# Performance work log

Measured on AMD Instinct MI355X. Metric: run time of the kernel, lower is better.

The kernel has to match this reference:

```python
import jax, jax.numpy as jnp
import numpy as np

NODE_DIM = 256
HID = 128
EDGE_DIM = 128
NUM_BINS = 22
MAX_LEN = 2056
TOTAL_FEATS = HID * 3 + NUM_BINS * 2 + 2


def get_index_embedding(indices, embed_size, max_len):
    # sinusoidal index embedding as in RiboFlow utils
    K = jnp.arange(embed_size // 2, dtype=jnp.float32)
    ang = indices[..., None].astype(jnp.float32) * jnp.pi / (max_len ** (2.0 * K / embed_size))
    return jnp.concatenate([jnp.sin(ang), jnp.cos(ang)], axis=-1)


def calc_distogram(pos, min_bin, max_bin, num_bins):
    # pos: [B, N, 3] -> one-hot distogram [B, N, N, num_bins]
    d = jnp.linalg.norm(pos[:, :, None, :] - pos[:, None, :, :], axis=-1)[..., None]
    lower = jnp.linspace(min_bin, max_bin, num_bins)
    upper = jnp.concatenate([lower[1:], jnp.array([1e8], dtype=jnp.float32)])
    return ((d > lower) & (d < upper)).astype(jnp.float32)


def cross_concat(f):
    # f: [B, N, D] -> [B, N, N, 2D] via row/col tiling
    B, N, D = f.shape
    return jnp.concatenate([
        jnp.broadcast_to(f[:, :, None, :], (B, N, N, D)),
        jnp.broadcast_to(f[:, None, :, :], (B, N, N, D)),
    ], axis=-1)


def _linear_params(key, fi, fo):
    s = 1.0 / np.sqrt(fi)
    kw, kb = jax.random.split(key)
    W = jax.random.uniform(kw, (fi, fo), jnp.float32, -s, s)
    b = jax.random.uniform(kb, (fo,), jnp.float32, -s, s)
    return W, b


def setup_inputs() -> dict:
    key = jax.random.key(0)
    ks = jax.random.split(key, 12)
    B, N = 1, 512
    inp = {
        'node_features': jax.random.normal(ks[0], (B, N, NODE_DIM), jnp.float32),
        'trans': jax.random.normal(ks[1], (B, N, 3), jnp.float32) * 10.0,
        'sc_trans': jax.random.normal(ks[2], (B, N, 3), jnp.float32) * 10.0,
        'edge_mask': jnp.ones((B, N, N), jnp.float32),
        'flow_mask': (jax.random.uniform(ks[4], (B, N)) > 0.5).astype(jnp.float32),
    }
    inp['W_n2e'], inp['b_n2e'] = _linear_params(ks[5], NODE_DIM, HID)
    inp['W_rp'], inp['b_rp'] = _linear_params(ks[6], HID, HID)
    inp['W1'], inp['b1'] = _linear_params(ks[7], TOTAL_FEATS, EDGE_DIM)
    inp['W2'], inp['b2'] = _linear_params(ks[8], EDGE_DIM, EDGE_DIM)
    inp['W3'], inp['b3'] = _linear_params(ks[9], EDGE_DIM, EDGE_DIM)
    inp['ln_g'] = jnp.ones((EDGE_DIM,), jnp.float32)
    inp['ln_b'] = jnp.zeros((EDGE_DIM,), jnp.float32)
    return inp


def reference(node_features, trans, sc_trans, edge_mask, flow_mask,
              W_n2e, b_n2e, W_rp, b_rp, W1, b1, W2, b2, W3, b3, ln_g, ln_b):
    B, N, _ = node_features.shape
    # node -> edge projection, then cross-concat tiling: [B,N,N,2*HID]
    n2e = node_features @ W_n2e + b_n2e
    pair_node_feats = cross_concat(n2e)
    # relative position sinusoidal embedding + linear: [B,N,N,HID]
    seq = jnp.arange(N, dtype=jnp.float32)
    relpos = jnp.broadcast_to(seq[None, :, None] - seq[None, None, :], (B, N, N))
    relpos_feats = get_index_embedding(relpos, HID, MAX_LEN) @ W_rp + b_rp
    # distograms: [B,N,N,NUM_BINS] each
    dist_feats = calc_distogram(trans, 0.001, 20.0, NUM_BINS)
    sc_feats = calc_distogram(sc_trans, 0.001, 20.0, NUM_BINS)
    # flow mask pair features: [B,N,N,2]
    flow_feat = cross_concat(flow_mask[..., None])
    feats = jnp.concatenate([pair_node_feats, relpos_feats, dist_feats, sc_feats, flow_feat], axis=-1)
    # 3-layer MLP + LayerNorm
    h = jax.nn.relu(feats @ W1 + b1)
    h = jax.nn.relu(h @ W2 + b2)
    h = h @ W3 + b3
    mu = jnp.mean(h, axis=-1, keepdims=True)
    var = jnp.var(h, axis=-1, keepdims=True)
    h = (h - mu) * jax.lax.rsqrt(var + 1e-5) * ln_g + ln_b
    return h * edge_mask[..., None]
```

## Files before the change

kernel.cpp:

```cpp
#include <hip/hip_runtime.h>


using bf16x8 = __attribute__((ext_vector_type(8))) short;
using f32x4  = __attribute__((ext_vector_type(4))) float;

__device__ __forceinline__ unsigned short f2bf(float f) {
    unsigned int u;
    __builtin_memcpy(&u, &f, 4);
    unsigned int r = (u + 0x7fffu + ((u >> 16) & 1u)) >> 16;
    return (unsigned short)r;
}

__global__ void pre_node(const float* __restrict__ nf,
                         const float* __restrict__ Wn2e,
                         const float* __restrict__ bn2e,
                         const float* __restrict__ W1,
                         const float* __restrict__ b1,
                         const float* __restrict__ flow,
                         float* __restrict__ A, float* __restrict__ Bv)
{
    __shared__ float nfs[256];
    __shared__ float n2s[128];
    const int i = blockIdx.x, f = threadIdx.x;
    nfs[f]       = nf[i * 256 + f];
    nfs[f + 128] = nf[i * 256 + 128 + f];
    __syncthreads();
    float acc = bn2e[f];
    for (int k = 0; k < 256; k++) acc += nfs[k] * Wn2e[k * 128 + f];
    n2s[f] = acc;
    __syncthreads();
    const float fl = flow[i];
    float aA = b1[f] + fl * W1[428 * 128 + f];
    float aB =         fl * W1[429 * 128 + f];
    for (int k = 0; k < 128; k++) {
        const float s = n2s[k];
        aA += s * W1[k * 128 + f];
        aB += s * W1[(128 + k) * 128 + f];
    }
    A[i * 128 + f]  = aA;
    Bv[i * 128 + f] = aB;
}

__global__ void pre_rel(const float* __restrict__ Wrp,
                        const float* __restrict__ brp,
                        const float* __restrict__ W1,
                        float* __restrict__ Rm)
{
    __shared__ float emb[128];
    __shared__ float rp[128];
    const int dix = blockIdx.x;
    const float d = (float)(dix - 511);
    const int m = threadIdx.x;
    const int K = m & 63;
    const float denom = powf(2056.0f, (float)K * (1.0f / 64.0f));
    const float ang = d * 3.14159265358979323846f / denom;
    emb[m] = (m < 64) ? sinf(ang) : cosf(ang);
    __syncthreads();
    float acc = brp[m];
    for (int k = 0; k < 128; k++) acc += emb[k] * Wrp[k * 128 + m];
    rp[m] = acc;
    __syncthreads();
    float acc2 = 0.0f;
    for (int k = 0; k < 128; k++) acc2 += rp[k] * W1[(256 + k) * 128 + m];
    Rm[dix * 128 + m] = acc2;
}

__global__ __launch_bounds__(512, 2) void edge_main(
    const float* __restrict__ trans,
    const float* __restrict__ sctrans,
    const float* __restrict__ emask,
    const float* __restrict__ W1,
    const float* __restrict__ W2,
    const float* __restrict__ b2,
    const float* __restrict__ W3,
    const float* __restrict__ b3,
    const float* __restrict__ lng,
    const float* __restrict__ lnb,
    const float* __restrict__ A,
    const float* __restrict__ Bv,
    const float* __restrict__ Rm,
    float* __restrict__ out)
{
    __shared__ __align__(16) short W2L[16 * 128 * 8];
    __shared__ __align__(16) short W3L[16 * 128 * 8];
    __shared__ __align__(16) short hbuf[256 * 136];
    __shared__ __align__(16) float As[128];
    __shared__ int binsD[256];
    __shared__ int binsS[256];

    const int tid = threadIdx.x;
    const int i  = blockIdx.x >> 1;
    const int j0 = (blockIdx.x & 1) << 8;

    for (int idx = tid; idx < 16384; idx += 512) {
        const int k = idx >> 7, n = idx & 127;
        const int dst = ((k >> 3) * 128 + n) * 8 + (k & 7);
        W2L[dst] = (short)f2bf(W2[idx]);
        W3L[dst] = (short)f2bf(W3[idx]);
    }
    if (tid < 128) As[tid] = A[i * 128 + tid];

    {
        const int p = tid & 255;
        const float* P = (tid < 256) ? trans : sctrans;
        const int j = j0 + p;
        const float dx = __fsub_rn(P[i * 3 + 0], P[j * 3 + 0]);
        const float dy = __fsub_rn(P[i * 3 + 1], P[j * 3 + 1]);
        const float dz = __fsub_rn(P[i * 3 + 2], P[j * 3 + 2]);
        const float d2 = __fadd_rn(__fadd_rn(__fmul_rn(dx, dx), __fmul_rn(dy, dy)),
                                   __fmul_rn(dz, dz));
        const double dd = (double)sqrtf(d2);
        const double step = (20.0 - 0.001) / 21.0;
        int bin = -1;
        for (int b = 0; b < 22; b++) {
            const double lo = (b == 21) ? 20.0 : __dadd_rn(0.001, __dmul_rn((double)b, step));
            const double up = (b == 20) ? 20.0 :
                              ((b == 21) ? 1e8 : __dadd_rn(0.001, __dmul_rn((double)(b + 1), step)));
            if (dd > lo && dd < up) bin = b;
        }
        if (tid < 256) binsD[p] = bin; else binsS[p] = bin;
    }
    __syncthreads();

    const int w = tid >> 6;
    const int l = tid & 63;
    const int q = l >> 4;
    const int ln16 = l & 15;

    for (int it = 0; it < 16; it++) {
        const int flat = it * 64 + l;
        const int p = 32 * w + (flat >> 5);
        const int f = (flat & 31) << 2;
        const int j = j0 + p;
        const int didx = i - j + 511;
        const f32x4 bv = *(const f32x4*)&Bv[j * 128 + f];
        const f32x4 r  = *(const f32x4*)&Rm[didx * 128 + f];
        const f32x4 a  = *(const f32x4*)&As[f];
        const int bD = binsD[p], bS = binsS[p];
        const float sD = bD >= 0 ? 1.0f : 0.0f;
        const float sS = bS >= 0 ? 1.0f : 0.0f;
        const int rD = 384 + (bD >= 0 ? bD : 0);
        const int rS = 406 + (bS >= 0 ? bS : 0);
        const f32x4 wd  = *(const f32x4*)&W1[rD * 128 + f];
        const f32x4 wsv = *(const f32x4*)&W1[rS * 128 + f];
        float h0 = a.x + bv.x + r.x + sD * wd.x + sS * wsv.x;
        float h1 = a.y + bv.y + r.y + sD * wd.y + sS * wsv.y;
        float h2 = a.z + bv.z + r.z + sD * wd.z + sS * wsv.z;
        float h3 = a.w + bv.w + r.w + sD * wd.w + sS * wsv.w;
        h0 = fmaxf(h0, 0.0f); h1 = fmaxf(h1, 0.0f);
        h2 = fmaxf(h2, 0.0f); h3 = fmaxf(h3, 0.0f);
        uint2 pk;
        pk.x = (unsigned int)f2bf(h0) | ((unsigned int)f2bf(h1) << 16);
        pk.y = (unsigned int)f2bf(h2) | ((unsigned int)f2bf(h3) << 16);
        *(uint2*)&hbuf[p * 136 + f] = pk;
    }
    __syncthreads();

    bf16x8 af[2][4];
    for (int mt = 0; mt < 2; mt++)
        for (int kb = 0; kb < 4; kb++)
            af[mt][kb] = *(const bf16x8*)&hbuf[(32 * w + mt * 16 + ln16) * 136 + q * 8 + kb * 32];

    const f32x4 vzero = {0.0f, 0.0f, 0.0f, 0.0f};
    f32x4 acc[2][8];
    for (int mt = 0; mt < 2; mt++)
        for (int nb = 0; nb < 8; nb++) acc[mt][nb] = vzero;

    for (int nb = 0; nb < 8; nb++) {
        for (int kb = 0; kb < 4; kb++) {
            const bf16x8 bfrg = *(const bf16x8*)&W2L[((kb * 4 + q) * 128 + nb * 16 + ln16) * 8];
            acc[0][nb] = __builtin_amdgcn_mfma_f32_16x16x32_bf16(af[0][kb], bfrg, acc[0][nb], 0, 0, 0);
            acc[1][nb] = __builtin_amdgcn_mfma_f32_16x16x32_bf16(af[1][kb], bfrg, acc[1][nb], 0, 0, 0);
        }
    }
    __syncthreads();

    float b2v[8];
    for (int nb = 0; nb < 8; nb++) b2v[nb] = b2[nb * 16 + ln16];
    for (int nb = 0; nb < 8; nb++)
        for (int mt = 0; mt < 2; mt++)
            for (int rg = 0; rg < 4; rg++) {
                float v = acc[mt][nb][rg] + b2v[nb];
                v = fmaxf(v, 0.0f);
                const int p = 32 * w + mt * 16 + q * 4 + rg;
                hbuf[p * 136 + nb * 16 + ln16] = (short)f2bf(v);
            }
    __syncthreads();

    for (int mt = 0; mt < 2; mt++)
        for (int kb = 0; kb < 4; kb++)
            af[mt][kb] = *(const bf16x8*)&hbuf[(32 * w + mt * 16 + ln16) * 136 + q * 8 + kb * 32];
    for (int mt = 0; mt < 2; mt++)
        for (int nb = 0; nb < 8; nb++) acc[mt][nb] = vzero;
    for (int nb = 0; nb < 8; nb++) {
        for (int kb = 0; kb < 4; kb++) {
            const bf16x8 bfrg = *(const bf16x8*)&W3L[((kb * 4 + q) * 128 + nb * 16 + ln16) * 8];
            acc[0][nb] = __builtin_amdgcn_mfma_f32_16x16x32_bf16(af[0][kb], bfrg, acc[0][nb], 0, 0, 0);
            acc[1][nb] = __builtin_amdgcn_mfma_f32_16x16x32_bf16(af[1][kb], bfrg, acc[1][nb], 0, 0, 0);
        }
    }

    float b3v[8], gv[8], bbv[8];
    for (int nb = 0; nb < 8; nb++) {
        const int n = nb * 16 + ln16;
        b3v[nb] = b3[n];
        gv[nb]  = lng[n];
        bbv[nb] = lnb[n];
    }
    for (int mt = 0; mt < 2; mt++) {
        for (int rg = 0; rg < 4; rg++) {
            float v[8];
            float s = 0.0f;
            for (int nb = 0; nb < 8; nb++) { v[nb] = acc[mt][nb][rg] + b3v[nb]; s += v[nb]; }
            for (int m = 1; m < 16; m <<= 1) s += __shfl_xor(s, m, 64);
            const float mu = s * (1.0f / 128.0f);
            float ss = 0.0f;
            for (int nb = 0; nb < 8; nb++) { const float dv = v[nb] - mu; ss += dv * dv; }
            for (int m = 1; m < 16; m <<= 1) ss += __shfl_xor(ss, m, 64);
            const float rstd = rsqrtf(ss * (1.0f / 128.0f) + 1e-5f);
            const int p = 32 * w + mt * 16 + q * 4 + rg;
            const int j = j0 + p;
            const float msk = emask[i * 512 + j];
            const int obase = (i * 512 + j) * 128;
            for (int nb = 0; nb < 8; nb++) {
                const float o = ((v[nb] - mu) * rstd * gv[nb] + bbv[nb]) * msk;
                out[obase + nb * 16 + ln16] = o;
            }
        }
    }
}

extern "C" void kernel_launch(void* const* d_in, const int* in_sizes, int n_in,
                              void* d_out, int out_size, void* d_ws, size_t ws_size,
                              hipStream_t stream)
{
    const float* nf    = (const float*)d_in[0];
    const float* trans = (const float*)d_in[1];
    const float* sctr  = (const float*)d_in[2];
    const float* emask = (const float*)d_in[3];
    const float* flow  = (const float*)d_in[4];
    const float* Wn2e  = (const float*)d_in[5];
    const float* bn2e  = (const float*)d_in[6];
    const float* Wrp   = (const float*)d_in[7];
    const float* brp   = (const float*)d_in[8];
    const float* W1    = (const float*)d_in[9];
    const float* b1    = (const float*)d_in[10];
    const float* W2    = (const float*)d_in[11];
    const float* b2    = (const float*)d_in[12];
    const float* W3    = (const float*)d_in[13];
    const float* b3    = (const float*)d_in[14];
    const float* lng   = (const float*)d_in[15];
    const float* lnb   = (const float*)d_in[16];

    float* ws = (float*)d_ws;
    float* A  = ws;
    float* Bv = ws + 512 * 128;
    float* Rm = ws + 2 * 512 * 128;
    float* out = (float*)d_out;

    pre_node<<<512, 128, 0, stream>>>(nf, Wn2e, bn2e, W1, b1, flow, A, Bv);
    pre_rel<<<1023, 128, 0, stream>>>(Wrp, brp, W1, Rm);
    edge_main<<<1024, 512, 0, stream>>>(trans, sctr, emask, W1, W2, b2, W3, b3,
                                        lng, lnb, A, Bv, Rm, out);
}
```

Measured before the change: 260.5 us.

## Precast W2/W3 to bf16 once, read from global, drop block syncs

Moves the per-block fp32-to-bf16 conversion and swizzle of W2/W3 into a merged precompute kernel, so edge_main reads pre-swizzled bf16 weights from global memory instead of staging them in LDS. The freed LDS and a per-warp row ownership that removes __syncthreads allow more blocks per CU (launch bounds raised to 4). It also merges the two pre kernels into one launch, replaces the 22-iteration double bin loop with a direct computation, and uses cheaper round-half-up bf16 packing. The direct bin formula and the rounding change may differ from the reference at bin edges.

After: 267.3 us. 2.6% more time.

```diff
diff --git a/kernel.cpp b/kernel.cpp
--- a/kernel.cpp
+++ b/kernel.cpp
@@ -4,138 +4,142 @@
 using bf16x8 = __attribute__((ext_vector_type(8))) short;
 using f32x4  = __attribute__((ext_vector_type(4))) float;
 
-__device__ __forceinline__ unsigned short f2bf(float f) {
-    unsigned int u;
-    __builtin_memcpy(&u, &f, 4);
-    unsigned int r = (u + 0x7fffu + ((u >> 16) & 1u)) >> 16;
-    return (unsigned short)r;
-}
-
-__global__ void pre_node(const float* __restrict__ nf,
-                         const float* __restrict__ Wn2e,
-                         const float* __restrict__ bn2e,
-                         const float* __restrict__ W1,
-                         const float* __restrict__ b1,
-                         const float* __restrict__ flow,
-                         float* __restrict__ A, float* __restrict__ Bv)
+__device__ __forceinline__ unsigned int fbits(float f) {
+    unsigned int u; __builtin_memcpy(&u, &f, 4); return u;
+}
+__device__ __forceinline__ unsigned short f2bf_rne(float f) {
+    unsigned int u = fbits(f);
+    return (unsigned short)((u + 0x7fffu + ((u >> 16) & 1u)) >> 16);
+}
+__device__ __forceinline__ unsigned short f2bf_rhu(float f) {
+    return (unsigned short)((fbits(f) + 0x8000u) >> 16);
+}
+
+__global__ void pre_all(const float* __restrict__ nf,
+                        const float* __restrict__ Wn2e,
+                        const float* __restrict__ bn2e,
+                        const float* __restrict__ W1,
+                        const float* __restrict__ b1,
+                        const float* __restrict__ flow,
+                        const float* __restrict__ Wrp,
+                        const float* __restrict__ brp,
+                        const float* __restrict__ W2,
+                        const float* __restrict__ W3,
+                        float* __restrict__ A, float* __restrict__ Bv,
+                        float* __restrict__ Rm,
+                        unsigned short* __restrict__ W2F,
+                        unsigned short* __restrict__ W3F)
 {
-    __shared__ float nfs[256];
-    __shared__ float n2s[128];
-    const int i = blockIdx.x, f = threadIdx.x;
-    nfs[f]       = nf[i * 256 + f];
-    nfs[f + 128] = nf[i * 256 + 128 + f];
-    __syncthreads();
-    float acc = bn2e[f];
-    for (int k = 0; k < 256; k++) acc += nfs[k] * Wn2e[k * 128 + f];
-    n2s[f] = acc;
-    __syncthreads();
-    const float fl = flow[i];
-    float aA = b1[f] + fl * W1[428 * 128 + f];
-    float aB =         fl * W1[429 * 128 + f];
-    for (int k = 0; k < 128; k++) {
-        const float s = n2s[k];
-        aA += s * W1[k * 128 + f];
-        aB += s * W1[(128 + k) * 128 + f];
-    }
-    A[i * 128 + f]  = aA;
-    Bv[i * 128 + f] = aB;
-}
-
-__global__ void pre_rel(const float* __restrict__ Wrp,
-                        const float* __restrict__ brp,
-                        const float* __restrict__ W1,
-                        float* __restrict__ Rm)
-{
-    __shared__ float emb[128];
-    __shared__ float rp[128];
-    const int dix = blockIdx.x;
-    const float d = (float)(dix - 511);
-    const int m = threadIdx.x;
-    const int K = m & 63;
-    const float denom = powf(2056.0f, (float)K * (1.0f / 64.0f));
-    const float ang = d * 3.14159265358979323846f / denom;
-    emb[m] = (m < 64) ? sinf(ang) : cosf(ang);
-    __syncthreads();
-    float acc = brp[m];
-    for (int k = 0; k < 128; k++) acc += emb[k] * Wrp[k * 128 + m];
-    rp[m] = acc;
-    __syncthreads();
-    float acc2 = 0.0f;
-    for (int k = 0; k < 128; k++) acc2 += rp[k] * W1[(256 + k) * 128 + m];
-    Rm[dix * 128 + m] = acc2;
-}
-
-__global__ __launch_bounds__(512, 2) void edge_main(
+    const int bid = blockIdx.x;
+    const int t = threadIdx.x;
+    if (bid < 512) {
+        __shared__ float nfs[256];
+        __shared__ float n2s[128];
+        const int i = bid;
+        nfs[t]       = nf[i * 256 + t];
+        nfs[t + 128] = nf[i * 256 + 128 + t];
+        __syncthreads();
+        float acc = bn2e[t];
+        for (int k = 0; k < 256; k++) acc += nfs[k] * Wn2e[k * 128 + t];
+        n2s[t] = acc;
+        __syncthreads();
+        const float fl = flow[i];
+        float aA = b1[t] + fl * W1[428 * 128 + t];
+        float aB =         fl * W1[429 * 128 + t];
+        for (int k = 0; k < 128; k++) {
+            const float s = n2s[k];
+            aA += s * W1[k * 128 + t];
+            aB += s * W1[(128 + k) * 128 + t];
+        }
+        A[i * 128 + t]  = aA;
+        Bv[i * 128 + t] = aB;
+    } else if (bid < 1535) {
+        __shared__ float emb[128];
+        __shared__ float rp[128];
+        const int dix = bid - 512;
+        const float d = (float)(dix - 511);
+        const int K = t & 63;
+        const float denom = powf(2056.0f, (float)K * (1.0f / 64.0f));
+        const float ang = d * 3.14159265358979323846f / denom;
+        emb[t] = (t < 64) ? sinf(ang) : cosf(ang);
+        __syncthreads();
+        float acc = brp[t];
+        for (int k = 0; k < 128; k++) acc += emb[k] * Wrp[k * 128 + t];
+        rp[t] = acc;
+        __syncthreads();
+        float acc2 = 0.0f;
+        for (int k = 0; k < 128; k++) acc2 += rp[k] * W1[(256 + k) * 128 + t];
+        Rm[dix * 128 + t] = acc2;
+    } else {
+        const int tg = (bid - 1535) * 128 + t;
+        for (int e = 0; e < 8; e++) {
+            const int idx = tg + e * 2048;
+            const int k = idx >> 7, n = idx & 127;
+            const int dst = ((k >> 3) * 128 + n) * 8 + (k & 7);
+            W2F[dst] = f2bf_rne(W2[idx]);
+            W3F[dst] = f2bf_rne(W3[idx]);
+        }
+    }
+}
+
+__global__ __launch_bounds__(512, 4) void edge_main(
     const float* __restrict__ trans,
     const float* __restrict__ sctrans,
     const float* __restrict__ emask,
     const float* __restrict__ W1,
-    const float* __restrict__ W2,
     const float* __restrict__ b2,
-    const float* __restrict__ W3,
     const float* __restrict__ b3,
     const float* __restrict__ lng,
     const float* __restrict__ lnb,
     const float* __restrict__ A,
     const float* __restrict__ Bv,
     const float* __restrict__ Rm,
+    const unsigned short* __restrict__ W2F,
+    const unsigned short* __restrict__ W3F,
     float* __restrict__ out)
 {
-    __shared__ __align__(16) short W2L[16 * 128 * 8];
-    __shared__ __align__(16) short W3L[16 * 128 * 8];
     __shared__ __align__(16) short hbuf[256 * 136];
-    __shared__ __align__(16) float As[128];
     __shared__ int binsD[256];
     __shared__ int binsS[256];
 
     const int tid = threadIdx.x;
     const int i  = blockIdx.x >> 1;
     const int j0 = (blockIdx.x & 1) << 8;
-
-    for (int idx = tid; idx < 16384; idx += 512) {
-        const int k = idx >> 7, n = idx & 127;
-        const int dst = ((k >> 3) * 128 + n) * 8 + (k & 7);
-        W2L[dst] = (short)f2bf(W2[idx]);
-        W3L[dst] = (short)f2bf(W3[idx]);
-    }
-    if (tid < 128) As[tid] = A[i * 128 + tid];
+    const int w = tid >> 6;
+    const int l = tid & 63;
+    const int q = l >> 4;
+    const int ln16 = l & 15;
+    const int row0 = 32 * w;
 
     {
-        const int p = tid & 255;
-        const float* P = (tid < 256) ? trans : sctrans;
+        const int pl = l & 31;
+        const int p = row0 + pl;
         const int j = j0 + p;
+        const float* P = (l < 32) ? trans : sctrans;
         const float dx = __fsub_rn(P[i * 3 + 0], P[j * 3 + 0]);
         const float dy = __fsub_rn(P[i * 3 + 1], P[j * 3 + 1]);
         const float dz = __fsub_rn(P[i * 3 + 2], P[j * 3 + 2]);
         const float d2 = __fadd_rn(__fadd_rn(__fmul_rn(dx, dx), __fmul_rn(dy, dy)),
                                    __fmul_rn(dz, dz));
         const double dd = (double)sqrtf(d2);
-        const double step = (20.0 - 0.001) / 21.0;
         int bin = -1;
-        for (int b = 0; b < 22; b++) {
-            const double lo = (b == 21) ? 20.0 : __dadd_rn(0.001, __dmul_rn((double)b, step));
-            const double up = (b == 20) ? 20.0 :
-                              ((b == 21) ? 1e8 : __dadd_rn(0.001, __dmul_rn((double)(b + 1), step)));
-            if (dd > lo && dd < up) bin = b;
-        }
-        if (tid < 256) binsD[p] = bin; else binsS[p] = bin;
-    }
-    __syncthreads();
-
-    const int w = tid >> 6;
-    const int l = tid & 63;
-    const int q = l >> 4;
-    const int ln16 = l & 15;
+        if (dd > 20.0) bin = 21;
+        else if (dd > 0.001) {
+            int b = (int)((dd - 0.001) * (21.0 / 19.999));
+            bin = (b > 20) ? 20 : b;
+        }
+        if (l < 32) binsD[p] = bin; else binsS[p] = bin;
+    }
 
     for (int it = 0; it < 16; it++) {
         const int flat = it * 64 + l;
-        const int p = 32 * w + (flat >> 5);
+        const int p = row0 + (flat >> 5);
         const int f = (flat & 31) << 2;
         const int j = j0 + p;
         const int didx = i - j + 511;
         const f32x4 bv = *(const f32x4*)&Bv[j * 128 + f];
         const f32x4 r  = *(const f32x4*)&Rm[didx * 128 + f];
-        const f32x4 a  = *(const f32x4*)&As[f];
+        const f32x4 a  = *(const f32x4*)&A[i * 128 + f];
         const int bD = binsD[p], bS = binsS[p];
         const float sD = bD >= 0 ? 1.0f : 0.0f;
         const float sS = bS >= 0 ? 1.0f : 0.0f;
@@ -150,81 +154,65 @@
         h0 = fmaxf(h0, 0.0f); h1 = fmaxf(h1, 0.0f);
         h2 = fmaxf(h2, 0.0f); h3 = fmaxf(h3, 0.0f);
         uint2 pk;
-        pk.x = (unsigned int)f2bf(h0) | ((unsigned int)f2bf(h1) << 16);
-        pk.y = (unsigned int)f2bf(h2) | ((unsigned int)f2bf(h3) << 16);
+        pk.x = ((fbits(h0) + 0x8000u) >> 16) | ((fbits(h1) + 0x8000u) & 0xffff0000u);
+        pk.y = ((fbits(h2) + 0x8000u) >> 16) | ((fbits(h3) + 0x8000u) & 0xffff0000u);
         *(uint2*)&hbuf[p * 136 + f] = pk;
     }
-    __syncthreads();
-
-    bf16x8 af[2][4];
-    for (int mt = 0; mt < 2; mt++)
-        for (int kb = 0; kb < 4; kb++)
-            af[mt][kb] = *(const bf16x8*)&hbuf[(32 * w + mt * 16 + ln16) * 136 + q * 8 + kb * 32];
 
     const f32x4 vzero = {0.0f, 0.0f, 0.0f, 0.0f};
-    f32x4 acc[2][8];
-    for (int mt = 0; mt < 2; mt++)
-        for (int nb = 0; nb < 8; nb++) acc[mt][nb] = vzero;
-
-    for (int nb = 0; nb < 8; nb++) {
-        for (int kb = 0; kb < 4; kb++) {
-            const bf16x8 bfrg = *(const bf16x8*)&W2L[((kb * 4 + q) * 128 + nb * 16 + ln16) * 8];
-            acc[0][nb] = __builtin_amdgcn_mfma_f32_16x16x32_bf16(af[0][kb], bfrg, acc[0][nb], 0, 0, 0);
-            acc[1][nb] = __builtin_amdgcn_mfma_f32_16x16x32_bf16(af[1][kb], bfrg, acc[1][nb], 0, 0, 0);
-        }
-    }
-    __syncthreads();
-
     float b2v[8];
     for (int nb = 0; nb < 8; nb++) b2v[nb] = b2[nb * 16 + ln16];
-    for (int nb = 0; nb < 8; nb++)
-        for (int mt = 0; mt < 2; mt++)
+
+    for (int mt = 0; mt < 2; mt++) {
+        bf16x8 af[4];
+        for (int kb = 0; kb < 4; kb++)
+            af[kb] = *(const bf16x8*)&hbuf[(row0 + mt * 16 + ln16) * 136 + q * 8 + kb * 32];
+        f32x4 acc[8];
+        for (int nb = 0; nb < 8; nb++) acc[nb] = vzero;
+        for (int nb = 0; nb < 8; nb++)
+            for (int kb = 0; kb < 4; kb++) {
+                const bf16x8 bfrg = *(const bf16x8*)&W2F[((kb * 4 + q) * 128 + nb * 16 + ln16) * 8];
+                acc[nb] = __builtin_amdgcn_mfma_f32_16x16x32_bf16(af[kb], bfrg, acc[nb], 0, 0, 0);
+            }
+        for (int nb = 0; nb < 8; nb++)
             for (int rg = 0; rg < 4; rg++) {
-                float v = acc[mt][nb][rg] + b2v[nb];
-                v = fmaxf(v, 0.0f);
-                const int p = 32 * w + mt * 16 + q * 4 + rg;
-                hbuf[p * 136 + nb * 16 + ln16] = (short)f2bf(v);
-            }
-    __syncthreads();
-
-    for (int mt = 0; mt < 2; mt++)
-        for (int kb = 0; kb < 4; kb++)
-            af[mt][kb] = *(const bf16x8*)&hbuf[(32 * w + mt * 16 + ln16) * 136 + q * 8 + kb * 32];
-    for (int mt = 0; mt < 2; mt++)
-        for (int nb = 0; nb < 8; nb++) acc[mt][nb] = vzero;
-    for (int nb = 0; nb < 8; nb++) {
-        for (int kb = 0; kb < 4; kb++) {
-            const bf16x8 bfrg = *(const bf16x8*)&W3L[((kb * 4 + q) * 128 + nb * 16 + ln16) * 8];
-            acc[0][nb] = __builtin_amdgcn_mfma_f32_16x16x32_bf16(af[0][kb], bfrg, acc[0][nb], 0, 0, 0);
-            acc[1][nb] = __builtin_amdgcn_mfma_f32_16x16x32_bf16(af[1][kb], bfrg, acc[1][nb], 0, 0, 0);
-        }
+                const float v = fmaxf(acc[nb][rg] + b2v[nb], 0.0f);
+                hbuf[(row0 + mt * 16 + q * 4 + rg) * 136 + nb * 16 + ln16] = (short)f2bf_rhu(v);
+            }
     }
 
     float b3v[8], gv[8], bbv[8];
     for (int nb = 0; nb < 8; nb++) {
         const int n = nb * 16 + ln16;
-        b3v[nb] = b3[n];
-        gv[nb]  = lng[n];
-        bbv[nb] = lnb[n];
+        b3v[nb] = b3[n]; gv[nb] = lng[n]; bbv[nb] = lnb[n];
     }
     for (int mt = 0; mt < 2; mt++) {
+        bf16x8 af[4];
+        for (int kb = 0; kb < 4; kb++)
+            af[kb] = *(const bf16x8*)&hbuf[(row0 + mt * 16 + ln16) * 136 + q * 8 + kb * 32];
+        f32x4 acc[8];
+        for (int nb = 0; nb < 8; nb++) acc[nb] = vzero;
+        for (int nb = 0; nb < 8; nb++)
+            for (int kb = 0; kb < 4; kb++) {
+                const bf16x8 bfrg = *(const bf16x8*)&W3F[((kb * 4 + q) * 128 + nb * 16 + ln16) * 8];
+                acc[nb] = __builtin_amdgcn_mfma_f32_16x16x32_bf16(af[kb], bfrg, acc[nb], 0, 0, 0);
+            }
         for (int rg = 0; rg < 4; rg++) {
             float v[8];
             float s = 0.0f;
-            for (int nb = 0; nb < 8; nb++) { v[nb] = acc[mt][nb][rg] + b3v[nb]; s += v[nb]; }
+            for (int nb = 0; nb < 8; nb++) { v[nb] = acc[nb][rg] + b3v[nb]; s += v[nb]; }
             for (int m = 1; m < 16; m <<= 1) s += __shfl_xor(s, m, 64);
             const float mu = s * (1.0f / 128.0f);
             float ss = 0.0f;
             for (int nb = 0; nb < 8; nb++) { const float dv = v[nb] - mu; ss += dv * dv; }
             for (int m = 1; m < 16; m <<= 1) ss += __shfl_xor(ss, m, 64);
             const float rstd = rsqrtf(ss * (1.0f / 128.0f) + 1e-5f);
-            const int p = 32 * w + mt * 16 + q * 4 + rg;
+            const int p = row0 + mt * 16 + q * 4 + rg;
             const int j = j0 + p;
             const float msk = emask[i * 512 + j];
             const int obase = (i * 512 + j) * 128;
             for (int nb = 0; nb < 8; nb++) {
-                const float o = ((v[nb] - mu) * rstd * gv[nb] + bbv[nb]) * msk;
-                out[obase + nb * 16 + ln16] = o;
+                out[obase + nb * 16 + ln16] = ((v[nb] - mu) * rstd * gv[nb] + bbv[nb]) * msk;
             }
         }
     }
@@ -256,10 +244,12 @@
     float* A  = ws;
     float* Bv = ws + 512 * 128;
     float* Rm = ws + 2 * 512 * 128;
+    unsigned short* W2F = (unsigned short*)(ws + 2 * 512 * 128 + 1023 * 128);
+    unsigned short* W3F = W2F + 16384;
     float* out = (float*)d_out;
 
-    pre_node<<<512, 128, 0, stream>>>(nf, Wn2e, bn2e, W1, b1, flow, A, Bv);
-    pre_rel<<<1023, 128, 0, stream>>>(Wrp, brp, W1, Rm);
-    edge_main<<<1024, 512, 0, stream>>>(trans, sctr, emask, W1, W2, b2, W3, b3,
-                                        lng, lnb, A, Bv, Rm, out);
-}
+    pre_all<<<1551, 128, 0, stream>>>(nf, Wn2e, bn2e, W1, b1, flow, Wrp, brp,
+                                      W2, W3, A, Bv, Rm, W2F, W3F);
+    edge_main<<<1024, 512, 0, stream>>>(trans, sctr, emask, W1, b2, b3,
+                                        lng, lnb, A, Bv, Rm, W2F, W3F, out);
+}
```
